# Performance work log

Hardware: AMD Instinct MI355X
Metric: run time of the kernel (lower is better)

Reference implementation:

```python
import jax, jax.numpy as jnp
import numpy as np


def setup_inputs() -> dict:
    key = jax.random.key(0)
    ks = jax.random.split(key, 8)
    Bsz, Dm, L, N = 2, 2048, 1024, 16
    u = jax.random.normal(ks[0], (Bsz, Dm, L), jnp.float32)
    delta = jax.random.normal(ks[1], (Bsz, Dm, L), jnp.float32) * 0.5
    # A is negative in Mamba (stable decay); keep values O(1) negative
    A = -jnp.exp(jax.random.normal(ks[2], (Dm, N), jnp.float32) * 0.5)
    B = jax.random.normal(ks[3], (Bsz, N, L), jnp.float32)
    C = jax.random.normal(ks[4], (Bsz, N, L), jnp.float32)
    D = jax.random.normal(ks[5], (Dm,), jnp.float32)
    z = jax.random.normal(ks[6], (Bsz, Dm, L), jnp.float32)
    delta_bias = jax.random.normal(ks[7], (Dm,), jnp.float32) * 0.1
    return {"u": u, "delta": delta, "A": A, "B": B, "C": C,
            "D": D, "z": z, "delta_bias": delta_bias, "delta_softplus": 1}


def reference(u, delta, A, B, C, D, z, delta_bias, delta_softplus):
    # u, delta, z: (Bsz, Dm, L); A: (Dm, N); B, C: (Bsz, N, L)
    dt = delta + delta_bias[None, :, None]
    if delta_softplus:
        dt = jax.nn.softplus(dt)

    # move scan (length) axis to the front
    dt_l = jnp.moveaxis(dt, -1, 0)   # (L, Bsz, Dm)
    u_l = jnp.moveaxis(u, -1, 0)     # (L, Bsz, Dm)
    B_l = jnp.moveaxis(B, -1, 0)     # (L, Bsz, N)
    C_l = jnp.moveaxis(C, -1, 0)     # (L, Bsz, N)

    def step(x, inp):
        dti, ui, Bi, Ci = inp
        dA = jnp.exp(dti[..., None] * A)                  # (Bsz, Dm, N)
        dBu = (dti * ui)[..., None] * Bi[:, None, :]      # (Bsz, Dm, N)
        x = dA * x + dBu
        y = jnp.einsum('bdn,bn->bd', x, Ci)               # (Bsz, Dm)
        return x, y

    x0 = jnp.zeros((u.shape[0], u.shape[1], A.shape[1]), dtype=u.dtype)
    _, ys = jax.lax.scan(step, x0, (dt_l, u_l, B_l, C_l))  # ys: (L, Bsz, Dm)
    y = jnp.moveaxis(ys, 0, -1)                            # (Bsz, Dm, L)
    y = y + u * D[None, :, None]
    y = y * (z * jax.nn.sigmoid(z))  # silu gate
    return y
```

## Files before the change

### kernel.cpp

```cpp
#include <hip/hip_runtime.h>
#include <math.h>

constexpr int Bsz = 2, Dm = 2048, L = 1024, N = 16;
constexpr int CL = 16;
constexpr int WPR = 2;
constexpr int RPB = 4;
constexpr int TPB = RPB * WPR * 64;
constexpr int NT = 8;
constexpr int ISTR2 = 65;
constexpr int LROW2 = CL * ISTR2;
constexpr int TS2 = 8 * 65;
constexpr float LOG2E = 1.4426950408889634f;
constexpr float RLOG2E = 0.6931471805599453f;

#define EXP2(x) __builtin_amdgcn_exp2f(x)

typedef __attribute__((ext_vector_type(2))) float f32x2;

__device__ __forceinline__ f32x2 pk_fma(f32x2 a, f32x2 b, f32x2 c) {
    return __builtin_elementwise_fma(a, b, c);
}

__device__ __forceinline__ void wg_barrier() {
    asm volatile("s_waitcnt lgkmcnt(0)" ::: "memory");
    __builtin_amdgcn_s_barrier();
    asm volatile("" ::: "memory");
}

__global__ __launch_bounds__(256) void transform_bc_kernel(
    const float* __restrict__ B_g, const float* __restrict__ C_g,
    float4* __restrict__ Bs, float4* __restrict__ Cs)
{
    const int o = threadIdx.x + 256 * blockIdx.x;
    const int b = blockIdx.y;
    const float* __restrict__ src = blockIdx.z ? C_g : B_g;
    float4* __restrict__ dst = blockIdx.z ? Cs : Bs;
    const int cg = o & 63, k = (o >> 6) & 3, i = o >> 8;
    const int l = cg * CL + i;
    float4 v;
    v.x = src[(size_t)(b * N + 4 * k + 0) * L + l];
    v.y = src[(size_t)(b * N + 4 * k + 1) * L + l];
    v.z = src[(size_t)(b * N + 4 * k + 2) * L + l];
    v.w = src[(size_t)(b * N + 4 * k + 3) * L + l];
    dst[(size_t)b * 4096 + o] = v;
}

template<bool XF>
__global__ __launch_bounds__(TPB) void mamba_scan21_kernel(
    const float* __restrict__ u_g, const float* __restrict__ delta_g,
    const float* __restrict__ A_g,
    const float* __restrict__ B_g, const float* __restrict__ C_g,
    const float4* __restrict__ Bs, const float4* __restrict__ Cs,
    const float* __restrict__ D_g, const float* __restrict__ z_g,
    const float* __restrict__ bias_g, const int* __restrict__ sp_g,
    float* __restrict__ y_g)
{
    __shared__ float2 du_s[RPB * LROW2];
    __shared__ float2 tb2[2][2 * TS2];
    __shared__ float xw_s[RPB][16];

    const int tid = threadIdx.x;
    const int wid = tid >> 6;
    const int lane = tid & 63;
    const int W = wid & 1;
    const int r = wid >> 1;
    const int h = lane >> 5;
    const int c = lane & 31;
    const int cg = W * 32 + c;
    const int row = blockIdx.x * RPB + r;
    const int b = row >> 11;
    const int d = row & (Dm - 1);
    const size_t Bb = (size_t)b * 4096;
    const int lb = r * LROW2;
    const int t128 = tid & 127;
    const int stg0 = (wid >> 2) * TS2 + (2 * (wid & 3)) * 65 + lane;
    const int stg1 = stg0 + 65;
    const int bc = tid >> 8;
    const int t256 = tid & 255;
    const int pstg0 = bc * TS2 + (2 * ((t256 >> 6) & 3)) * 65 + (t256 & 63);
    const int pstg1 = pstg0 + 65;
    const float4* __restrict__ psrc = (bc ? Cs : Bs) + Bb;
    const int trb = (4 * h) * 65 + cg;

    float4 s0, s1;
    if (XF) s0 = Bs[Bb + tid];

    {
        const float bias = bias_g[d];
        const int sp = sp_g[0];
#pragma unroll
        for (int p = 0; p < 2; ++p) {
            const int l0 = 4 * t128 + 512 * p;
            const size_t gb = (size_t)row * L + l0;
            const float4 d4 = *reinterpret_cast<const float4*>(&delta_g[gb]);
            const float4 u4 = *reinterpret_cast<const float4*>(&u_g[gb]);
#pragma unroll
            for (int k = 0; k < 4; ++k) {
                const int li = l0 + k;
                const float t = (&d4.x)[k] + bias;
                const float e = EXP2(-fabsf(t) * LOG2E);
                const float p_ = sp ? (fmaxf(t, 0.f) +
                                       __builtin_amdgcn_logf(1.f + e) * RLOG2E)
                                    : t;
                const int a = (li & (CL - 1)) * ISTR2 + (li >> 4);
                du_s[lb + a] = make_float2(p_, (&u4.x)[k]);
            }
        }
    }
    float A2[8];
    f32x2 A2p[4];
#pragma unroll
    for (int g = 0; g < 2; ++g) {
        const float4 a4 = *reinterpret_cast<const float4*>(&A_g[d * N + h * 8 + g * 4]);
        A2[g * 4 + 0] = a4.x * LOG2E; A2[g * 4 + 1] = a4.y * LOG2E;
        A2[g * 4 + 2] = a4.z * LOG2E; A2[g * 4 + 3] = a4.w * LOG2E;
    }
#pragma unroll
    for (int q = 0; q < 4; ++q) { A2p[q].x = A2[2 * q]; A2p[q].y = A2[2 * q + 1]; }
    if (XF) {
        tb2[0][stg0] = make_float2(s0.x, s0.y);
        tb2[0][stg1] = make_float2(s0.z, s0.w);
        s0 = Bs[Bb + 512 + tid];
        s1 = Bs[Bb + 1024 + tid];
    }
    wg_barrier();

    f32x2 x2[4];
#pragma unroll
    for (int q = 0; q < 4; ++q) { x2[q].x = 0.f; x2[q].y = 0.f; }
    float y[8];
#pragma unroll
    for (int n = 0; n < 8; ++n) y[n] = 0.f;
    float ssum = 0.f;

    if (XF) {
#pragma unroll
        for (int t = 0; t < NT; ++t) {
#pragma unroll
            for (int il = 0; il < 2; ++il) {
                const int i = 2 * t + il;
                const float2 du = du_s[lb + i * ISTR2 + cg];
                const float dtp = du.x;
                const float dtu = du.x * du.y;
                ssum += dtp;
                const int rb = il * TS2 + trb;
                f32x2 qv[4];
                qv[0] = *reinterpret_cast<const f32x2*>(&tb2[t & 1][rb]);
                qv[1] = *reinterpret_cast<const f32x2*>(&tb2[t & 1][rb + 65]);
                qv[2] = *reinterpret_cast<const f32x2*>(&tb2[t & 1][rb + 130]);
                qv[3] = *reinterpret_cast<const f32x2*>(&tb2[t & 1][rb + 195]);
                f32x2 dd; dd.x = dtp; dd.y = dtp;
                f32x2 uu2; uu2.x = dtu; uu2.y = dtu;
#pragma unroll
                for (int q = 0; q < 4; ++q) {
                    const f32x2 tq = dd * A2p[q];
                    f32x2 e; e.x = EXP2(tq.x); e.y = EXP2(tq.y);
                    const f32x2 db = uu2 * qv[q];
                    x2[q] = pk_fma(e, x2[q], db);
                }
            }
            if (t + 1 < NT) {
                const float4 sv = (t & 1) ? s1 : s0;
                tb2[(t + 1) & 1][stg0] = make_float2(sv.x, sv.y);
                tb2[(t + 1) & 1][stg1] = make_float2(sv.z, sv.w);
            }
            if (t + 3 < NT) {
                if (t & 1) s1 = Bs[Bb + (t + 3) * 512 + tid];
                else       s0 = Bs[Bb + (t + 3) * 512 + tid];
            }
            if (t + 1 < NT) wg_barrier();
        }
    } else {
#pragma unroll
        for (int i = 0; i < CL; ++i) {
            const float2 du = du_s[lb + i * ISTR2 + cg];
            const float dtp = du.x;
            const float dtu = du.x * du.y;
            ssum += dtp;
            const int l = cg * CL + i;
            const int k0 = 2 * h;
            float4 B0, B1;
#pragma unroll
            for (int q = 0; q < 4; ++q) {
                (&B0.x)[q] = B_g[(size_t)(b * N + 4 * k0 + q) * L + l];
                (&B1.x)[q] = B_g[(size_t)(b * N + 4 * k0 + 4 + q) * L + l];
            }
            const float bv[8] = {B0.x, B0.y, B0.z, B0.w, B1.x, B1.y, B1.z, B1.w};
#pragma unroll
            for (int n = 0; n < 8; ++n) {
                const float a = EXP2(dtp * A2[n]);
                const float xs = (n & 1) ? x2[n >> 1].y : x2[n >> 1].x;
                const float xn = fmaf(a, xs, dtu * bv[n]);
                if (n & 1) x2[n >> 1].y = xn; else x2[n >> 1].x = xn;
            }
        }
    }

    float x[8];
#pragma unroll
    for (int q = 0; q < 4; ++q) { x[2 * q] = x2[q].x; x[2 * q + 1] = x2[q].y; }

    float4 p0, p1;
    if (XF) p0 = psrc[t256];

    float P[8];
#pragma unroll
    for (int n = 0; n < 8; ++n) P[n] = EXP2(A2[n] * ssum);
#pragma unroll
    for (int s = 1; s < 32; s <<= 1) {
        const bool ok = (c >= s);
#pragma unroll
        for (int n = 0; n < 8; ++n) {
            const float xp = __shfl_up(x[n], s, 32);
            const float Pp = __shfl_up(P[n], s, 32);
            if (ok) {
                x[n] = fmaf(P[n], xp, x[n]);
                P[n] = P[n] * Pp;
            }
        }
    }

    if (W == 0 && c == 31) {
#pragma unroll
        for (int n = 0; n < 8; ++n) xw_s[r][h * 8 + n] = x[n];
    }
    if (XF) {
        tb2[0][pstg0] = make_float2(p0.x, p0.y);
        tb2[0][pstg1] = make_float2(p0.z, p0.w);
        p0 = psrc[1 * 256 + t256];
        p1 = psrc[2 * 256 + t256];
    }
    wg_barrier();

    float xt[8];
#pragma unroll
    for (int n = 0; n < 8; ++n) xt[n] = xw_s[r][h * 8 + n];
#pragma unroll
    for (int n = 0; n < 8; ++n) {
        const float xi = __shfl_up(x[n], 1, 32);
        const float Pi = __shfl_up(P[n], 1, 32);
        const float xe = (c == 0) ? 0.f : xi;
        const float Pe = (c == 0) ? 1.f : Pi;
        x[n] = W ? fmaf(Pe, xt[n], xe) : xe;
    }

#pragma unroll
    for (int q = 0; q < 4; ++q) { x2[q].x = x[2 * q]; x2[q].y = x[2 * q + 1]; }

    const float Dd = D_g[d];
    if (XF) {
#pragma unroll
        for (int i = 0; i < CL; ++i) {
            const float2 du = du_s[lb + i * ISTR2 + cg];
            const float dtp = du.x;
            const float uu = du.y;
            const float dtu = dtp * uu;
            f32x2 qb[4], qc[4];
            qb[0] = *reinterpret_cast<const f32x2*>(&tb2[i & 1][trb]);
            qb[1] = *reinterpret_cast<const f32x2*>(&tb2[i & 1][trb + 65]);
            qb[2] = *reinterpret_cast<const f32x2*>(&tb2[i & 1][trb + 130]);
            qb[3] = *reinterpret_cast<const f32x2*>(&tb2[i & 1][trb + 195]);
            qc[0] = *reinterpret_cast<const f32x2*>(&tb2[i & 1][TS2 + trb]);
            qc[1] = *reinterpret_cast<const f32x2*>(&tb2[i & 1][TS2 + trb + 65]);
            qc[2] = *reinterpret_cast<const f32x2*>(&tb2[i & 1][TS2 + trb + 130]);
            qc[3] = *reinterpret_cast<const f32x2*>(&tb2[i & 1][TS2 + trb + 195]);
            f32x2 dd; dd.x = dtp; dd.y = dtp;
            f32x2 uu2; uu2.x = dtu; uu2.y = dtu;
            f32x2 acc2; acc2.x = 0.f; acc2.y = 0.f;
#pragma unroll
            for (int q = 0; q < 4; ++q) {
                const f32x2 tq = dd * A2p[q];
                f32x2 e; e.x = EXP2(tq.x); e.y = EXP2(tq.y);
                const f32x2 db = uu2 * qb[q];
                x2[q] = pk_fma(e, x2[q], db);
                acc2 = pk_fma(x2[q], qc[q], acc2);
            }
            float acc = acc2.x + acc2.y;
            acc += __shfl_xor(acc, 32, 64);
            const float yv = fmaf(uu, Dd, acc);
            y[i & 7] = ((i >> 3) == h) ? yv : y[i & 7];
            if (i + 1 < CL) {
                const float4 pv = (i & 1) ? p1 : p0;
                tb2[(i + 1) & 1][pstg0] = make_float2(pv.x, pv.y);
                tb2[(i + 1) & 1][pstg1] = make_float2(pv.z, pv.w);
            }
            if (i + 3 < CL) {
                if (i & 1) p1 = psrc[(i + 3) * 256 + t256];
                else       p0 = psrc[(i + 3) * 256 + t256];
            }
            if (i + 1 < CL) wg_barrier();
        }
    } else {
#pragma unroll
        for (int i = 0; i < CL; ++i) {
            const float2 du = du_s[lb + i * ISTR2 + cg];
            const float dtp = du.x;
            const float uu = du.y;
            const float dtu = dtp * uu;
            const int l = cg * CL + i;
            const int k0 = 2 * h;
            float4 B0, B1, C0, C1;
#pragma unroll
            for (int q = 0; q < 4; ++q) {
                (&B0.x)[q] = B_g[(size_t)(b * N + 4 * k0 + q) * L + l];
                (&B1.x)[q] = B_g[(size_t)(b * N + 4 * k0 + 4 + q) * L + l];
                (&C0.x)[q] = C_g[(size_t)(b * N + 4 * k0 + q) * L + l];
                (&C1.x)[q] = C_g[(size_t)(b * N + 4 * k0 + 4 + q) * L + l];
            }
            const float bv[8] = {B0.x, B0.y, B0.z, B0.w, B1.x, B1.y, B1.z, B1.w};
            const float cv[8] = {C0.x, C0.y, C0.z, C0.w, C1.x, C1.y, C1.z, C1.w};
            float acc = 0.f;
#pragma unroll
            for (int n = 0; n < 8; ++n) {
                const float a = EXP2(dtp * A2[n]);
                const float xs = (n & 1) ? x2[n >> 1].y : x2[n >> 1].x;
                const float xn = fmaf(a, xs, dtu * bv[n]);
                if (n & 1) x2[n >> 1].y = xn; else x2[n >> 1].x = xn;
                acc = fmaf(xn, cv[n], acc);
            }
            acc += __shfl_xor(acc, 32, 64);
            const float yv = fmaf(uu, Dd, acc);
            y[i & 7] = ((i >> 3) == h) ? yv : y[i & 7];
        }
    }

    {
        const size_t gz = (size_t)row * L + cg * CL + h * 8;
        const float4 z0 = *reinterpret_cast<const float4*>(&z_g[gz]);
        const float4 z1 = *reinterpret_cast<const float4*>(&z_g[gz + 4]);
        float out[8];
#pragma unroll
        for (int j = 0; j < 8; ++j) {
            const float zv = (j < 4) ? (&z0.x)[j] : (&z1.x)[j - 4];
            const float e = EXP2(-zv * LOG2E);
            const float sig = __builtin_amdgcn_rcpf(1.f + e);
            out[j] = y[j] * (zv * sig);
        }
        *reinterpret_cast<float4*>(&y_g[gz]) =
            make_float4(out[0], out[1], out[2], out[3]);
        *reinterpret_cast<float4*>(&y_g[gz + 4]) =
            make_float4(out[4], out[5], out[6], out[7]);
    }
}

extern "C" void kernel_launch(void* const* d_in, const int* in_sizes, int n_in,
                              void* d_out, int out_size, void* d_ws, size_t ws_size,
                              hipStream_t stream) {
    const float* u     = (const float*)d_in[0];
    const float* delta = (const float*)d_in[1];
    const float* A     = (const float*)d_in[2];
    const float* B     = (const float*)d_in[3];
    const float* C     = (const float*)d_in[4];
    const float* D     = (const float*)d_in[5];
    const float* z     = (const float*)d_in[6];
    const float* bias  = (const float*)d_in[7];
    const int*   sp    = (const int*)d_in[8];
    float* y = (float*)d_out;

    const size_t bc_bytes = (size_t)Bsz * 4096 * sizeof(float4);
    const bool xf = ws_size >= 2 * bc_bytes;
    float4* Bs = (float4*)d_ws;
    float4* Cs = (float4*)((char*)d_ws + bc_bytes);

    if (xf) {
        transform_bc_kernel<<<dim3(16, Bsz, 2), 256, 0, stream>>>(B, C, Bs, Cs);
        mamba_scan21_kernel<true><<<dim3((Bsz * Dm) / RPB), TPB, 0, stream>>>(
            u, delta, A, B, C, Bs, Cs, D, z, bias, sp, y);
    } else {
        mamba_scan21_kernel<false><<<dim3((Bsz * Dm) / RPB), TPB, 0, stream>>>(
            u, delta, A, B, C, Bs, Cs, D, z, bias, sp, y);
    }
}
```

Baseline: 46.29 us.

## Replace shuffle-based chunk scan with DPP combine tracking summed delta

The cross-lane prefix scan over chunk states now uses DPP row_shr and row_bcast15 moves instead of __shfl_up. Instead of carrying per-state decay products P[n], it carries a single summed delta and recomputes each decay as exp2(A*ss), which removes half the cross-lane traffic. The exclusive shift is also done with DPP. The cost is extra exp2 evaluations in each stage in exchange for fewer ds_bpermute operations, and the fallback path's B/C loads are reorganized.

```diff
diff --git a/kernel.cpp b/kernel.cpp
--- a/kernel.cpp
+++ b/kernel.cpp
@@ -20,6 +20,19 @@
 __device__ __forceinline__ f32x2 pk_fma(f32x2 a, f32x2 b, f32x2 c) {
     return __builtin_elementwise_fma(a, b, c);
 }
+
+#define DPPF(CTRL, RM, v) __builtin_bit_cast(float, __builtin_amdgcn_update_dpp( \
+        0, __builtin_bit_cast(int, (float)(v)), (CTRL), (RM), 0xF, false))
+
+#define COMBINE_STAGE(CTRL, RM) do {                                      \
+    const float ssp_ = DPPF(CTRL, RM, ss);                                \
+    float xp_[8];                                                         \
+    _Pragma("unroll") for (int n_ = 0; n_ < 8; ++n_)                      \
+        xp_[n_] = DPPF(CTRL, RM, x[n_]);                                  \
+    _Pragma("unroll") for (int n_ = 0; n_ < 8; ++n_)                      \
+        x[n_] = fmaf(EXP2(A2[n_] * ss), xp_[n_], x[n_]);                  \
+    ss += ssp_;                                                           \
+} while (0)
 
 __device__ __forceinline__ void wg_barrier() {
     asm volatile("s_waitcnt lgkmcnt(0)" ::: "memory");
@@ -46,7 +59,7 @@
 }
 
 template<bool XF>
-__global__ __launch_bounds__(TPB) void mamba_scan21_kernel(
+__global__ __launch_bounds__(TPB) void mamba_scan23_kernel(
     const float* __restrict__ u_g, const float* __restrict__ delta_g,
     const float* __restrict__ A_g,
     const float* __restrict__ B_g, const float* __restrict__ C_g,
@@ -131,7 +144,7 @@
     float y[8];
 #pragma unroll
     for (int n = 0; n < 8; ++n) y[n] = 0.f;
-    float ssum = 0.f;
+    float ss = 0.f;
 
     if (XF) {
 #pragma unroll
@@ -142,7 +155,7 @@
                 const float2 du = du_s[lb + i * ISTR2 + cg];
                 const float dtp = du.x;
                 const float dtu = du.x * du.y;
-                ssum += dtp;
+                ss += dtp;
                 const int rb = il * TS2 + trb;
                 f32x2 qv[4];
                 qv[0] = *reinterpret_cast<const f32x2*>(&tb2[t & 1][rb]);
@@ -176,7 +189,7 @@
             const float2 du = du_s[lb + i * ISTR2 + cg];
             const float dtp = du.x;
             const float dtu = du.x * du.y;
-            ssum += dtp;
+            ss += dtp;
             const int l = cg * CL + i;
             const int k0 = 2 * h;
             float4 B0, B1;
@@ -203,22 +216,11 @@
     float4 p0, p1;
     if (XF) p0 = psrc[t256];
 
-    float P[8];
-#pragma unroll
-    for (int n = 0; n < 8; ++n) P[n] = EXP2(A2[n] * ssum);
-#pragma unroll
-    for (int s = 1; s < 32; s <<= 1) {
-        const bool ok = (c >= s);
-#pragma unroll
-        for (int n = 0; n < 8; ++n) {
-            const float xp = __shfl_up(x[n], s, 32);
-            const float Pp = __shfl_up(P[n], s, 32);
-            if (ok) {
-                x[n] = fmaf(P[n], xp, x[n]);
-                P[n] = P[n] * Pp;
-            }
-        }
-    }
+    COMBINE_STAGE(0x111, 0xF);
+    COMBINE_STAGE(0x112, 0xF);
+    COMBINE_STAGE(0x114, 0xF);
+    COMBINE_STAGE(0x118, 0xF);
+    COMBINE_STAGE(0x142, 0xA);
 
     if (W == 0 && c == 31) {
 #pragma unroll
@@ -232,16 +234,20 @@
     }
     wg_barrier();
 
-    float xt[8];
-#pragma unroll
-    for (int n = 0; n < 8; ++n) xt[n] = xw_s[r][h * 8 + n];
-#pragma unroll
-    for (int n = 0; n < 8; ++n) {
-        const float xi = __shfl_up(x[n], 1, 32);
-        const float Pi = __shfl_up(P[n], 1, 32);
-        const float xe = (c == 0) ? 0.f : xi;
-        const float Pe = (c == 0) ? 1.f : Pi;
-        x[n] = W ? fmaf(Pe, xt[n], xe) : xe;
+    {
+        float xt[8];
+#pragma unroll
+        for (int n = 0; n < 8; ++n) xt[n] = xw_s[r][h * 8 + n];
+        const float ss1 = DPPF(0x111, 0xF, ss);
+        const float ssb = DPPF(0x142, 0xA, ss);
+        const float sse = (c == 16) ? ssb : ss1;
+#pragma unroll
+        for (int n = 0; n < 8; ++n) {
+            const float x1 = DPPF(0x111, 0xF, x[n]);
+            const float xb = DPPF(0x142, 0xA, x[n]);
+            const float xe = (c == 16) ? xb : x1;
+            x[n] = W ? fmaf(EXP2(A2[n] * sse), xt[n], xe) : xe;
+        }
     }
 
 #pragma unroll
@@ -299,16 +305,12 @@
             const float dtu = dtp * uu;
             const int l = cg * CL + i;
             const int k0 = 2 * h;
-            float4 B0, B1, C0, C1;
-#pragma unroll
-            for (int q = 0; q < 4; ++q) {
-                (&B0.x)[q] = B_g[(size_t)(b * N + 4 * k0 + q) * L + l];
-                (&B1.x)[q] = B_g[(size_t)(b * N + 4 * k0 + 4 + q) * L + l];
-                (&C0.x)[q] = C_g[(size_t)(b * N + 4 * k0 + q) * L + l];
-                (&C1.x)[q] = C_g[(size_t)(b * N + 4 * k0 + 4 + q) * L + l];
-            }
-            const float bv[8] = {B0.x, B0.y, B0.z, B0.w, B1.x, B1.y, B1.z, B1.w};
-            const float cv[8] = {C0.x, C0.y, C0.z, C0.w, C1.x, C1.y, C1.z, C1.w};
+            float bv[8], cv[8];
+#pragma unroll
+            for (int q = 0; q < 8; ++q) {
+                bv[q] = B_g[(size_t)(b * N + 4 * k0 + q) * L + l];
+                cv[q] = C_g[(size_t)(b * N + 4 * k0 + q) * L + l];
+            }
             float acc = 0.f;
 #pragma unroll
             for (int n = 0; n < 8; ++n) {
@@ -364,10 +366,10 @@
 
     if (xf) {
         transform_bc_kernel<<<dim3(16, Bsz, 2), 256, 0, stream>>>(B, C, Bs, Cs);
-        mamba_scan21_kernel<true><<<dim3((Bsz * Dm) / RPB), TPB, 0, stream>>>(
+        mamba_scan23_kernel<true><<<dim3((Bsz * Dm) / RPB), TPB, 0, stream>>>(
             u, delta, A, B, C, Bs, Cs, D, z, bias, sp, y);
     } else {
-        mamba_scan21_kernel<false><<<dim3((Bsz * Dm) / RPB), TPB, 0, stream>>>(
+        mamba_scan23_kernel<false><<<dim3((Bsz * Dm) / RPB), TPB, 0, stream>>>(
             u, delta, A, B, C, Bs, Cs, D, z, bias, sp, y);
     }
 }
```

Result: faster. 43.21 us (-6.7%).
